# Performance work log

Measured on AMD Instinct MI355X. Metric: run time of the kernel, lower is better.

Reference implementation:

```python
import jax, jax.numpy as jnp
import numpy as np

B, S, NCH, OUT = 16384, 256, 8, 2
EPS = 1e-5

def setup_inputs() -> dict:
    key = jax.random.key(0)
    ks = jax.random.split(key, 8)
    scale = 1.0 / np.sqrt(S)
    x = jax.random.normal(ks[0], (B, S, 2 * NCH), dtype=jnp.float32)
    h_0 = jnp.zeros((1,), dtype=jnp.float32)
    # per-channel complex linear weights, stacked: [n_channels, out=S, in=S]
    Wr = jax.random.normal(ks[1], (NCH, S, S), dtype=jnp.float32) * scale
    Wi = jax.random.normal(ks[2], (NCH, S, S), dtype=jnp.float32) * scale
    # final complex linear: [out=OUT//2, in=NCH*S]
    Wfr = jax.random.normal(ks[3], (OUT // 2, NCH * S), dtype=jnp.float32) / np.sqrt(NCH * S)
    Wfi = jax.random.normal(ks[4], (OUT // 2, NCH * S), dtype=jnp.float32) / np.sqrt(NCH * S)
    g_in = jnp.ones((2 * NCH,), dtype=jnp.float32)
    b_in = jnp.zeros((2 * NCH,), dtype=jnp.float32)
    g_out = jnp.ones((OUT,), dtype=jnp.float32)
    b_out = jnp.zeros((OUT,), dtype=jnp.float32)
    return {"x": x, "h_0": h_0, "Wr": Wr, "Wi": Wi, "Wfr": Wfr, "Wfi": Wfi,
            "g_in": g_in, "b_in": b_in, "g_out": g_out, "b_out": b_out}

def reference(x, h_0, Wr, Wi, Wfr, Wfi, g_in, b_in, g_out, b_out):
    # bn_in (training mode): x permuted to [B, 2n, S] in torch -> stats per feature over (B, S)
    mu = jnp.mean(x, axis=(0, 1))
    var = jnp.var(x, axis=(0, 1))  # biased, as torch uses for normalization
    xn = (x - mu) * jax.lax.rsqrt(var + EPS) * g_in + b_in  # [B, S, 2n]
    xi = xn[:, :, 0::2]  # [B, S, n] real parts
    xq = xn[:, :, 1::2]  # [B, S, n] imag parts
    # batched complex linear over channels: y[b,o,c] = sum_s x[b,s,c] W[c,o,s]
    cr = jnp.einsum('bsc,cos->boc', xi, Wr) - jnp.einsum('bsc,cos->boc', xq, Wi)
    ci = jnp.einsum('bsc,cos->boc', xq, Wr) + jnp.einsum('bsc,cos->boc', xi, Wi)
    amp2 = xi * xi + xq * xq  # [B, S, n]
    # channel blocks concatenated along last dim: channel-major ordering
    x_ii = jnp.transpose(amp2 * cr, (0, 2, 1)).reshape(B, NCH * S)
    x_qq = jnp.transpose(amp2 * ci, (0, 2, 1)).reshape(B, NCH * S)
    Cr = x_ii @ Wfr.T - x_qq @ Wfi.T  # [B, OUT//2]
    Ci = x_qq @ Wfr.T + x_ii @ Wfi.T
    y = jnp.concatenate([Cr, Ci], axis=-1)  # [B, OUT]
    mu2 = jnp.mean(y, axis=0)
    var2 = jnp.var(y, axis=0)
    return (y - mu2) * jax.lax.rsqrt(var2 + EPS) * g_out + b_out
```

## Files before the change

kernel.cpp:

```cpp
#include <hip/hip_runtime.h>
#include <stdint.h>

#define B_N   16384
#define S_N   256
#define NCH   8
#define P_N   (B_N * S_N)
#define EPS_F 1e-5f

typedef float  f32x4  __attribute__((ext_vector_type(4)));
typedef float  f32x16 __attribute__((ext_vector_type(16)));
typedef __bf16 bf16x8 __attribute__((ext_vector_type(8)));
typedef unsigned int u32x4 __attribute__((ext_vector_type(4)));

static __device__ __forceinline__ unsigned short f2bf(float f) {
  union { float f; unsigned u; } v; v.f = f;
  unsigned u = v.u;
  u += 0x7fffu + ((u >> 16) & 1u);
  return (unsigned short)(u >> 16);
}
static __device__ __forceinline__ float bf2f(unsigned short h) {
  union { unsigned u; float f; } v; v.u = ((unsigned)h) << 16;
  return v.f;
}

typedef const __attribute__((address_space(1))) unsigned int* gas1_t;
typedef __attribute__((address_space(3))) unsigned int* las3_t;
static __device__ __forceinline__ void gl16(const void* g, void* l) {
  __builtin_amdgcn_global_load_lds((gas1_t)(uintptr_t)g,
                                   (las3_t)(unsigned int)(uintptr_t)l, 16, 0, 0);
}

__global__ __launch_bounds__(256) void pass1_kernel(
    const float* __restrict__ x, unsigned short* __restrict__ xplan,
    float* __restrict__ partials)
{
  __shared__ float ps[4][32];
  const int t = threadIdx.x;
  const int q = t & 3;
  const int pg = t >> 2;
  float s[4] = {0.f,0.f,0.f,0.f}, ss[4] = {0.f,0.f,0.f,0.f};
  const f32x4* xv = (const f32x4*)x;

  for (int it = 0; it < 4; ++it) {
    size_t p0 = ((size_t)blockIdx.x * 4 + it) * 512 + (size_t)pg * 8;
    f32x4 v[8];
    #pragma unroll
    for (int j = 0; j < 8; ++j) v[j] = xv[(p0 + j) * 4 + q];
    #pragma unroll
    for (int j = 0; j < 8; ++j)
      #pragma unroll
      for (int k = 0; k < 4; ++k) { s[k] += v[j][k]; ss[k] += v[j][k] * v[j][k]; }
    #pragma unroll
    for (int j2 = 0; j2 < 4; ++j2) {
      u32x4 w;
      #pragma unroll
      for (int k = 0; k < 4; ++k)
        w[k] = (unsigned)f2bf(v[2*k][j2]) | ((unsigned)f2bf(v[2*k+1][j2]) << 16);
      *(u32x4*)(xplan + (size_t)(q * 4 + j2) * P_N + p0) = w;
    }
  }

  #pragma unroll
  for (int off = 32; off >= 4; off >>= 1) {
    #pragma unroll
    for (int k = 0; k < 4; ++k) { s[k] += __shfl_down(s[k], off); ss[k] += __shfl_down(ss[k], off); }
  }
  const int lane = t & 63, wid = t >> 6;
  if (lane < 4) {
    #pragma unroll
    for (int k = 0; k < 4; ++k) {
      ps[wid][lane * 4 + k]      = s[k];
      ps[wid][16 + lane * 4 + k] = ss[k];
    }
  }
  __syncthreads();
  if (t < 32)
    partials[blockIdx.x * 32 + t] = ps[0][t] + ps[1][t] + ps[2][t] + ps[3][t];
}

__global__ __launch_bounds__(1024) void finalize_kernel(
    const float* __restrict__ partials, const float* __restrict__ g_in,
    const float* __restrict__ b_in, float* __restrict__ AC)
{
  __shared__ float acc[32][32];
  const int t = threadIdx.x;
  const int v = t & 31, chunk = t >> 5;
  float s = 0.f;
  for (int i = 0; i < 64; ++i)
    s += partials[(size_t)(chunk * 64 + i) * 32 + v];
  acc[chunk][v] = s;
  __syncthreads();
  if (t < 32) {
    float tot = 0.f;
    #pragma unroll
    for (int k = 0; k < 32; ++k) tot += acc[k][t];
    acc[0][t] = tot;
  }
  __syncthreads();
  if (t < 16) {
    float n = (float)P_N;
    float mu  = acc[0][t] / n;
    float var = acc[0][16 + t] / n - mu * mu;
    float A = g_in[t] * rsqrtf(var + EPS_F);
    AC[t] = A;
    AC[16 + t] = b_in[t] - mu * A;
  }
}

__global__ __launch_bounds__(256) void wprep_kernel(
    const float* __restrict__ Wr, const float* __restrict__ Wi,
    unsigned short* __restrict__ wrp, unsigned short* __restrict__ wip,
    float* __restrict__ RWr, float* __restrict__ RWi)
{
  __shared__ float sr[4], si[4];
  const int row = blockIdx.x, t = threadIdx.x;
  const int c = row >> 8, o = row & 255;
  const int ow = o >> 5, o31 = o & 31;
  const size_t idx = (size_t)row * 256 + t;
  float vr = Wr[idx], vi = Wi[idx];
  const int u = t >> 4, kh = (t >> 3) & 1, j = t & 7;
  const size_t widx = ((((size_t)(c * 8 + ow) * 16 + u) * 2 + kh) * 32 + o31) * 8 + j;
  wrp[widx] = f2bf(vr);
  wip[widx] = f2bf(vi);
  float rr = vr, ri = vi;
  #pragma unroll
  for (int off = 32; off >= 1; off >>= 1) { rr += __shfl_down(rr, off); ri += __shfl_down(ri, off); }
  if ((t & 63) == 0) { sr[t >> 6] = rr; si[t >> 6] = ri; }
  __syncthreads();
  if (t == 0) {
    RWr[row] = sr[0] + sr[1] + sr[2] + sr[3];
    RWi[row] = si[0] + si[1] + si[2] + si[3];
  }
}

__global__ __launch_bounds__(256) void kterm_kernel(
    const float* __restrict__ AC, const float* __restrict__ RWr, const float* __restrict__ RWi,
    float* __restrict__ Kr, float* __restrict__ Ki)
{
  int idx = blockIdx.x * 256 + threadIdx.x;
  int c = idx >> 8;
  float Ci_ = AC[16 + 2*c], Cq_ = AC[16 + 2*c + 1];
  Kr[idx] = Ci_ * RWr[idx] - Cq_ * RWi[idx];
  Ki[idx] = Cq_ * RWr[idx] + Ci_ * RWi[idx];
}

static __device__ __forceinline__ void stage_x(
    const unsigned short* __restrict__ xplan, int c, int r0, char* buf, int t)
{
  #pragma unroll
  for (int i = 0; i < 4; ++i) {
    const int pl = i >> 1;
    const int row = (i & 1) * 16 + (t >> 5);
    const int g = (t & 31) ^ (row & 7);
    const char* gsrc = (const char*)xplan +
      (((size_t)(2 * c + pl) * P_N + (size_t)(r0 + row) * 256 + g * 8) << 1);
    gl16(gsrc, buf + pl * 16384 + row * 512 + (t & 31) * 16);
  }
}

__global__ __launch_bounds__(512, 2) void main_kernel(
    const unsigned short* __restrict__ xplan,
    const unsigned short* __restrict__ wrp,
    const unsigned short* __restrict__ wip,
    const float* __restrict__ AC,
    const float* __restrict__ Kr, const float* __restrict__ Ki,
    const float* __restrict__ Wfr, const float* __restrict__ Wfi,
    float* __restrict__ pacc)
{
  __shared__ char X[2][32768];
  __shared__ float red[8][32][2];

  const int t = threadIdx.x;
  const int w = t >> 6, lane = t & 63;
  const int o31 = lane & 31, kh = lane >> 5;
  const int c = blockIdx.x & 7;
  const int b0 = (blockIdx.x >> 3) * 256;

  const int o = w * 32 + o31;
  const int gidx = c * 256 + o;
  const float kr = Kr[gidx], ki = Ki[gidx];
  const float wfr = Wfr[gidx], wfi = Wfi[gidx];
  const float Ai = AC[2*c], Aq = AC[2*c + 1];
  const float Ci = AC[16 + 2*c], Cq = AC[16 + 2*c + 1];

  bf16x8 wr8[16], wi8[16];
  {
    const char* wb  = (const char*)wrp + (size_t)(c * 8 + w) * 16384 + kh * 512 + o31 * 16;
    const char* wib = (const char*)wip + (size_t)(c * 8 + w) * 16384 + kh * 512 + o31 * 16;
    #pragma unroll
    for (int u = 0; u < 16; ++u) {
      wr8[u] = *(const bf16x8*)(wb  + u * 1024);
      wi8[u] = *(const bf16x8*)(wib + u * 1024);
    }
  }

  stage_x(xplan, c, b0, X[0], t);

  #pragma unroll 1
  for (int tile = 0; tile < 8; ++tile) {
    __builtin_amdgcn_s_barrier();
    if (tile + 1 < 8) {
      stage_x(xplan, c, b0 + (tile + 1) * 32, X[(tile + 1) & 1], t);
      asm volatile("s_waitcnt vmcnt(4)" ::: "memory");
    } else {
      asm volatile("s_waitcnt vmcnt(0)" ::: "memory");
    }
    __builtin_amdgcn_sched_barrier(0);

    const char* Xb = (const char*)X[tile & 1];
    f32x16 arr, aqr, ari, aqi;
    #pragma unroll
    for (int e = 0; e < 16; ++e) { arr[e]=0.f; aqr[e]=0.f; ari[e]=0.f; aqi[e]=0.f; }

    __builtin_amdgcn_s_setprio(1);
    #pragma unroll
    for (int u = 0; u < 16; ++u) {
      const int ga = (((u * 2 + kh) ^ (o31 & 7)) << 4);
      bf16x8 xi8 = *(const bf16x8*)(Xb + o31 * 512 + ga);
      bf16x8 xq8 = *(const bf16x8*)(Xb + 16384 + o31 * 512 + ga);
      arr = __builtin_amdgcn_mfma_f32_32x32x16_bf16(xi8, wr8[u], arr, 0,0,0);
      aqr = __builtin_amdgcn_mfma_f32_32x32x16_bf16(xq8, wr8[u], aqr, 0,0,0);
      ari = __builtin_amdgcn_mfma_f32_32x32x16_bf16(xi8, wi8[u], ari, 0,0,0);
      aqi = __builtin_amdgcn_mfma_f32_32x32x16_bf16(xq8, wi8[u], aqi, 0,0,0);
    }
    __builtin_amdgcn_s_setprio(0);

    #pragma unroll
    for (int q = 0; q < 16; ++q) {
      const int brow = (q & 3) + 8 * (q >> 2) + 4 * kh;
      const int ge = ((((o >> 3) ^ (brow & 7)) << 4)) + (o & 7) * 2;
      float xiv = Ai * bf2f(*(const unsigned short*)(Xb + brow * 512 + ge)) + Ci;
      float xqv = Aq * bf2f(*(const unsigned short*)(Xb + 16384 + brow * 512 + ge)) + Cq;
      float amp = xiv * xiv + xqv * xqv;
      float cr  = Ai * arr[q] - Aq * aqi[q] + kr;
      float ci_ = Aq * aqr[q] + Ai * ari[q] + ki;
      float p0 = amp * (cr * wfr - ci_ * wfi);
      float p1 = amp * (ci_ * wfr + cr * wfi);
      #pragma unroll
      for (int off = 1; off < 32; off <<= 1) {
        p0 += __shfl_xor(p0, off);
        p1 += __shfl_xor(p1, off);
      }
      if (o31 == 0) { red[w][brow][0] = p0; red[w][brow][1] = p1; }
    }
    __builtin_amdgcn_s_barrier();
    if (t < 64) {
      const int row = t >> 1, cc = t & 1;
      float v = 0.f;
      #pragma unroll
      for (int ww = 0; ww < 8; ++ww) v += red[ww][row][cc];
      pacc[((size_t)c * B_N + b0 + tile * 32 + row) * 2 + cc] = v;
    }
  }
}

__global__ __launch_bounds__(256) void ln_a_kernel(
    const float* __restrict__ pacc, float* __restrict__ y, float* __restrict__ spart)
{
  __shared__ float ws_[4][4];
  const int t = threadIdx.x;
  const int r = blockIdx.x * 256 + t;
  float v0 = 0.f, v1 = 0.f;
  #pragma unroll
  for (int c = 0; c < 8; ++c) {
    v0 += pacc[((size_t)c * B_N + r) * 2];
    v1 += pacc[((size_t)c * B_N + r) * 2 + 1];
  }
  y[r * 2] = v0; y[r * 2 + 1] = v1;
  float s0 = v0, q0 = v0 * v0, s1 = v1, q1 = v1 * v1;
  #pragma unroll
  for (int off = 32; off >= 1; off >>= 1) {
    s0 += __shfl_down(s0, off); q0 += __shfl_down(q0, off);
    s1 += __shfl_down(s1, off); q1 += __shfl_down(q1, off);
  }
  if ((t & 63) == 0) { int wv = t >> 6; ws_[wv][0]=s0; ws_[wv][1]=q0; ws_[wv][2]=s1; ws_[wv][3]=q1; }
  __syncthreads();
  if (t < 4)
    spart[blockIdx.x * 4 + t] = ws_[0][t] + ws_[1][t] + ws_[2][t] + ws_[3][t];
}

__global__ void ln_b_kernel(const float* __restrict__ spart, float* __restrict__ st)
{
  const int t = threadIdx.x;
  const int q = t & 3, i0 = t >> 2;
  float s = 0.f;
  #pragma unroll
  for (int i = 0; i < 4; ++i) s += spart[(i0 + i * 16) * 4 + q];
  s += __shfl_down(s, 32); s += __shfl_down(s, 16);
  s += __shfl_down(s, 8);  s += __shfl_down(s, 4);
  if (t < 4) {
    float n = (float)B_N;
    float S0 = __shfl(s, 0), Q0 = __shfl(s, 1), S1 = __shfl(s, 2), Q1 = __shfl(s, 3);
    if (t == 0) {
      float mu0 = S0 / n, var0 = Q0 / n - mu0 * mu0;
      float mu1 = S1 / n, var1 = Q1 / n - mu1 * mu1;
      st[0] = mu0; st[1] = rsqrtf(var0 + EPS_F);
      st[2] = mu1; st[3] = rsqrtf(var1 + EPS_F);
    }
  }
}

__global__ __launch_bounds__(256) void ln_c_kernel(
    const float* __restrict__ y, const float* __restrict__ st,
    const float* __restrict__ g_out, const float* __restrict__ b_out,
    float* __restrict__ out)
{
  const int i = blockIdx.x * 256 + threadIdx.x;
  const int cc = i & 1;
  out[i] = (y[i] - st[cc * 2]) * st[cc * 2 + 1] * g_out[cc] + b_out[cc];
}

extern "C" void kernel_launch(void* const* d_in, const int* in_sizes, int n_in,
                              void* d_out, int out_size, void* d_ws, size_t ws_size,
                              hipStream_t stream) {
  (void)in_sizes; (void)n_in; (void)out_size; (void)ws_size;
  const float* x    = (const float*)d_in[0];
  const float* Wr   = (const float*)d_in[2];
  const float* Wi   = (const float*)d_in[3];
  const float* Wfr  = (const float*)d_in[4];
  const float* Wfi  = (const float*)d_in[5];
  const float* g_in = (const float*)d_in[6];
  const float* b_in = (const float*)d_in[7];
  const float* g_out= (const float*)d_in[8];
  const float* b_out= (const float*)d_in[9];
  float* out = (float*)d_out;

  char* ws = (char*)d_ws;
  float* AC    = (float*)(ws + 128);
  float* RWr   = (float*)(ws + 256);
  float* RWi   = (float*)(ws + 8448);
  float* Kr    = (float*)(ws + 16640);
  float* Ki    = (float*)(ws + 24832);
  float* spart = (float*)(ws + 33024);
  float* st    = (float*)(ws + 34048);
  float* y     = (float*)(ws + 36864);
  unsigned short* wrp = (unsigned short*)(ws + 167936);
  unsigned short* wip = (unsigned short*)(ws + 167936 + 1048576);
  float* pacc  = (float*)(ws + 2265088);
  float* partials = (float*)(ws + 2265088);
  unsigned short* xplan = (unsigned short*)(ws + 3313664);

  pass1_kernel<<<2048, 256, 0, stream>>>(x, xplan, partials);
  finalize_kernel<<<1, 1024, 0, stream>>>(partials, g_in, b_in, AC);
  wprep_kernel<<<2048, 256, 0, stream>>>(Wr, Wi, wrp, wip, RWr, RWi);
  kterm_kernel<<<8, 256, 0, stream>>>(AC, RWr, RWi, Kr, Ki);
  main_kernel<<<512, 512, 0, stream>>>(xplan, wrp, wip, AC, Kr, Ki, Wfr, Wfi, pacc);
  ln_a_kernel<<<64, 256, 0, stream>>>(pacc, y, spart);
  ln_b_kernel<<<1, 64, 0, stream>>>(spart, st);
  ln_c_kernel<<<128, 256, 0, stream>>>(y, st, g_out, b_out, out);
}
```

Measured before the change: 238.6 us.

## Swap MFMA operands so batch rows map to lanes and drop shuffle reduction

Swaps the A/B operands of the MFMAs so each lane holds outputs for a single batch row across 16 output features. The epilogue can then accumulate per lane and needs only one cross-half shuffle, replacing the 5-step xor-shuffle tree per element. The per-feature K and final weights become 16-element register arrays. The LDS staging now uses a full XOR swizzle over 32 groups with linear thread-contiguous writes. The manual vmcnt waits and sched barriers are replaced by __syncthreads. This raises register pressure and may weaken the overlap between the prefetch and compute.

Result: slower. 342.1 us (+43.4%).

```diff
diff --git a/kernel.cpp b/kernel.cpp
--- a/kernel.cpp
+++ b/kernel.cpp
@@ -149,12 +149,12 @@
 {
   #pragma unroll
   for (int i = 0; i < 4; ++i) {
-    const int pl = i >> 1;
-    const int row = (i & 1) * 16 + (t >> 5);
-    const int g = (t & 31) ^ (row & 7);
+    const int rowp = i * 16 + (t >> 5);
+    const int pl = rowp >> 5, row = rowp & 31;
+    const int g = (t & 31) ^ row;
     const char* gsrc = (const char*)xplan +
       (((size_t)(2 * c + pl) * P_N + (size_t)(r0 + row) * 256 + g * 8) << 1);
-    gl16(gsrc, buf + pl * 16384 + row * 512 + (t & 31) * 16);
+    gl16(gsrc, buf + i * 8192 + t * 16);
   }
 }
 
@@ -172,21 +172,26 @@
 
   const int t = threadIdx.x;
   const int w = t >> 6, lane = t & 63;
-  const int o31 = lane & 31, kh = lane >> 5;
+  const int l31 = lane & 31, kh = lane >> 5;
   const int c = blockIdx.x & 7;
   const int b0 = (blockIdx.x >> 3) * 256;
 
-  const int o = w * 32 + o31;
-  const int gidx = c * 256 + o;
-  const float kr = Kr[gidx], ki = Ki[gidx];
-  const float wfr = Wfr[gidx], wfi = Wfi[gidx];
   const float Ai = AC[2*c], Aq = AC[2*c + 1];
   const float Ci = AC[16 + 2*c], Cq = AC[16 + 2*c + 1];
 
+  float kr[16], ki[16], fr[16], fi[16];
+  #pragma unroll
+  for (int q = 0; q < 16; ++q) {
+    const int o = w * 32 + (q & 3) + 8 * (q >> 2) + 4 * kh;
+    const int gidx = c * 256 + o;
+    kr[q] = Kr[gidx]; ki[q] = Ki[gidx];
+    fr[q] = Wfr[gidx]; fi[q] = Wfi[gidx];
+  }
+
   bf16x8 wr8[16], wi8[16];
   {
-    const char* wb  = (const char*)wrp + (size_t)(c * 8 + w) * 16384 + kh * 512 + o31 * 16;
-    const char* wib = (const char*)wip + (size_t)(c * 8 + w) * 16384 + kh * 512 + o31 * 16;
+    const char* wb  = (const char*)wrp + (size_t)(c * 8 + w) * 16384 + kh * 512 + l31 * 16;
+    const char* wib = (const char*)wip + (size_t)(c * 8 + w) * 16384 + kh * 512 + l31 * 16;
     #pragma unroll
     for (int u = 0; u < 16; ++u) {
       wr8[u] = *(const bf16x8*)(wb  + u * 1024);
@@ -195,17 +200,12 @@
   }
 
   stage_x(xplan, c, b0, X[0], t);
+  __syncthreads();
 
   #pragma unroll 1
   for (int tile = 0; tile < 8; ++tile) {
-    __builtin_amdgcn_s_barrier();
-    if (tile + 1 < 8) {
+    if (tile + 1 < 8)
       stage_x(xplan, c, b0 + (tile + 1) * 32, X[(tile + 1) & 1], t);
-      asm volatile("s_waitcnt vmcnt(4)" ::: "memory");
-    } else {
-      asm volatile("s_waitcnt vmcnt(0)" ::: "memory");
-    }
-    __builtin_amdgcn_sched_barrier(0);
 
     const char* Xb = (const char*)X[tile & 1];
     f32x16 arr, aqr, ari, aqi;
@@ -215,35 +215,34 @@
     __builtin_amdgcn_s_setprio(1);
     #pragma unroll
     for (int u = 0; u < 16; ++u) {
-      const int ga = (((u * 2 + kh) ^ (o31 & 7)) << 4);
-      bf16x8 xi8 = *(const bf16x8*)(Xb + o31 * 512 + ga);
-      bf16x8 xq8 = *(const bf16x8*)(Xb + 16384 + o31 * 512 + ga);
-      arr = __builtin_amdgcn_mfma_f32_32x32x16_bf16(xi8, wr8[u], arr, 0,0,0);
-      aqr = __builtin_amdgcn_mfma_f32_32x32x16_bf16(xq8, wr8[u], aqr, 0,0,0);
-      ari = __builtin_amdgcn_mfma_f32_32x32x16_bf16(xi8, wi8[u], ari, 0,0,0);
-      aqi = __builtin_amdgcn_mfma_f32_32x32x16_bf16(xq8, wi8[u], aqi, 0,0,0);
+      const int ga = (((u * 2 + kh) ^ l31) << 4);
+      bf16x8 xi8 = *(const bf16x8*)(Xb + l31 * 512 + ga);
+      bf16x8 xq8 = *(const bf16x8*)(Xb + 16384 + l31 * 512 + ga);
+      arr = __builtin_amdgcn_mfma_f32_32x32x16_bf16(wr8[u], xi8, arr, 0,0,0);
+      aqr = __builtin_amdgcn_mfma_f32_32x32x16_bf16(wr8[u], xq8, aqr, 0,0,0);
+      ari = __builtin_amdgcn_mfma_f32_32x32x16_bf16(wi8[u], xi8, ari, 0,0,0);
+      aqi = __builtin_amdgcn_mfma_f32_32x32x16_bf16(wi8[u], xq8, aqi, 0,0,0);
     }
     __builtin_amdgcn_s_setprio(0);
 
+    float pC0 = 0.f, pC1 = 0.f;
     #pragma unroll
     for (int q = 0; q < 16; ++q) {
-      const int brow = (q & 3) + 8 * (q >> 2) + 4 * kh;
-      const int ge = ((((o >> 3) ^ (brow & 7)) << 4)) + (o & 7) * 2;
-      float xiv = Ai * bf2f(*(const unsigned short*)(Xb + brow * 512 + ge)) + Ci;
-      float xqv = Aq * bf2f(*(const unsigned short*)(Xb + 16384 + brow * 512 + ge)) + Cq;
+      const int o = w * 32 + (q & 3) + 8 * (q >> 2) + 4 * kh;
+      const int sb = l31 * 512 + (((o >> 3) ^ l31) << 4) + (o & 7) * 2;
+      float xiv = Ai * bf2f(*(const unsigned short*)(Xb + sb)) + Ci;
+      float xqv = Aq * bf2f(*(const unsigned short*)(Xb + 16384 + sb)) + Cq;
       float amp = xiv * xiv + xqv * xqv;
-      float cr  = Ai * arr[q] - Aq * aqi[q] + kr;
-      float ci_ = Aq * aqr[q] + Ai * ari[q] + ki;
-      float p0 = amp * (cr * wfr - ci_ * wfi);
-      float p1 = amp * (ci_ * wfr + cr * wfi);
-      #pragma unroll
-      for (int off = 1; off < 32; off <<= 1) {
-        p0 += __shfl_xor(p0, off);
-        p1 += __shfl_xor(p1, off);
-      }
-      if (o31 == 0) { red[w][brow][0] = p0; red[w][brow][1] = p1; }
-    }
-    __builtin_amdgcn_s_barrier();
+      float cr  = Ai * arr[q] - Aq * aqi[q] + kr[q];
+      float ci_ = Aq * aqr[q] + Ai * ari[q] + ki[q];
+      pC0 += amp * (cr * fr[q] - ci_ * fi[q]);
+      pC1 += amp * (ci_ * fr[q] + cr * fi[q]);
+    }
+    pC0 += __shfl_xor(pC0, 32);
+    pC1 += __shfl_xor(pC1, 32);
+    if (lane < 32) { red[w][l31][0] = pC0; red[w][l31][1] = pC1; }
+
+    __syncthreads();
     if (t < 64) {
       const int row = t >> 1, cc = t & 1;
       float v = 0.f;
```
